# Kernel tuning notes

Hardware: AMD Instinct MI355X
Metric: run time of the kernel (lower is better)

Reference implementation:

```python
import jax, jax.numpy as jnp
import numpy as np

N = 10000      # num_nodes
E = 640000     # num edges
IN, HID, OUT = 128, 128, 128


def setup_inputs() -> dict:
    key = jax.random.key(0)
    k = jax.random.split(key, 7)
    node_features = jax.random.normal(k[0], (N, IN), dtype=jnp.float32)
    edge_index = jax.random.randint(k[1], (2, E), 0, N)
    edge_attributes = jax.random.uniform(k[2], (E,), dtype=jnp.float32)
    # GCNConv params: weight [in, out] (glorot-ish), bias [out] (zeros in PyG; use small random)
    W1 = jax.random.normal(k[3], (IN, HID), dtype=jnp.float32) * (1.0 / np.sqrt(IN))
    b1 = jnp.zeros((HID,), dtype=jnp.float32)
    W2 = jax.random.normal(k[4], (HID, OUT), dtype=jnp.float32) * (1.0 / np.sqrt(HID))
    b2 = jnp.zeros((OUT,), dtype=jnp.float32)
    return {"node_features": node_features, "edge_index": edge_index,
            "edge_attributes": edge_attributes, "W1": W1, "b1": b1, "W2": W2, "b2": b2}


def gcn_conv(x, edge_index, edge_weight, W, b, n):
    """PyG GCNConv: add self-loops (weight 1), symmetric deg^{-1/2} normalization,
    linear transform, scatter-add aggregation source->target, then bias."""
    xw = x @ W                                   # [n, out]
    row, col = edge_index[0], edge_index[1]
    loop = jnp.arange(n)
    row = jnp.concatenate([row, loop])
    col = jnp.concatenate([col, loop])
    w = jnp.concatenate([edge_weight, jnp.ones((n,), edge_weight.dtype)])
    deg = jax.ops.segment_sum(w, col, num_segments=n)
    deg_safe = jnp.where(deg > 0, deg, 1.0)
    dinv = jnp.where(deg > 0, jax.lax.rsqrt(deg_safe), 0.0)
    norm = dinv[row] * w * dinv[col]             # [E+n]
    out = jax.ops.segment_sum(norm[:, None] * xw[row], col, num_segments=n)
    return out + b


def reference(node_features, edge_index, edge_attributes, W1, b1, W2, b2):
    # Module replaces node_features with all-ones of shape (num_nodes, input_channels).
    x = jnp.ones((N, IN), dtype=node_features.dtype)
    x = jax.nn.relu(gcn_conv(x, edge_index, edge_attributes, W1, b1, N))
    x = gcn_conv(x, edge_index, edge_attributes, W2, b2, N)
    # global_mean_pool with batch=None -> mean over all nodes, shape [1, OUT]
    return jnp.mean(x, axis=0, keepdims=True)
```

## Files before the change

### kernel.cpp

```cpp
#include <hip/hip_runtime.h>

#define N_NODES 10000
#define E_EDGES 640000
#define C 128
#define NBA 128
#define NBS 128
#define NBC 63
#define CCH 160

typedef float vf4 __attribute__((ext_vector_type(4)));

__device__ __forceinline__ void lds_add(float* p, float v) {
    __hip_atomic_fetch_add(p, v, __ATOMIC_RELAXED, __HIP_MEMORY_SCOPE_WORKGROUP);
}

__global__ __launch_bounds__(512) void k_deg(const int* __restrict__ col,
                                             const float* __restrict__ w,
                                             float* __restrict__ degp) {
    __shared__ float sdeg[N_NODES];
    const int tid = threadIdx.x, bid = blockIdx.x;
    vf4 z = {0.f, 0.f, 0.f, 0.f};
    for (int i = tid; i < N_NODES / 4; i += 512) ((vf4*)sdeg)[i] = z;
    __syncthreads();
    const int epb = E_EDGES / NBA;
    const int4*   col4 = (const int4*)(col + bid * epb);
    const float4* w4   = (const float4*)(w + bid * epb);
    for (int k = tid; k < epb / 4; k += 512) {
        int4 cc = col4[k]; float4 ww = w4[k];
        lds_add(&sdeg[cc.x], ww.x);
        lds_add(&sdeg[cc.y], ww.y);
        lds_add(&sdeg[cc.z], ww.z);
        lds_add(&sdeg[cc.w], ww.w);
    }
    __syncthreads();
    float* dst = degp + (size_t)bid * N_NODES;
    for (int i = tid; i < N_NODES / 4; i += 512)
        ((vf4*)dst)[i] = ((const vf4*)sdeg)[i];
}

__global__ __launch_bounds__(256) void k_dinv(const float* __restrict__ degp,
                                              float* __restrict__ dinv,
                                              const float* __restrict__ W1,
                                              float* __restrict__ s1,
                                              float* __restrict__ g,
                                              unsigned* __restrict__ ctrl) {
    int i = blockIdx.x * 256 + threadIdx.x;
    if (i < N_NODES) {
        float d = 1.0f;
        #pragma unroll 16
        for (int b = 0; b < NBA; ++b) d += degp[(size_t)b * N_NODES + i];
        dinv[i] = rsqrtf(d);
    }
    if (blockIdx.x == 0) {
        if (threadIdx.x < C) {
            int j = threadIdx.x;
            float s = 0.0f;
            #pragma unroll 16
            for (int k = 0; k < C; ++k) s += W1[k * C + j];
            s1[j] = s;
            g[j]  = 0.0f;
        }
        if (threadIdx.x == 0) *ctrl = 0u;
    }
}

__global__ __launch_bounds__(512) void k_scatter(const int* __restrict__ row,
                                                 const int* __restrict__ col,
                                                 const float* __restrict__ w,
                                                 const float* __restrict__ dinv,
                                                 float* __restrict__ tap,
                                                 float* __restrict__ tbp) {
    __shared__ float st[N_NODES];
    const int tid = threadIdx.x;
    const bool isA = blockIdx.x < NBS;
    const int bid  = isA ? blockIdx.x : blockIdx.x - NBS;
    vf4 z = {0.f, 0.f, 0.f, 0.f};
    for (int i = tid; i < N_NODES / 4; i += 512) ((vf4*)st)[i] = z;
    __syncthreads();
    const int epb = E_EDGES / NBS;
    const int4*   row4 = (const int4*)(row + bid * epb);
    const int4*   col4 = (const int4*)(col + bid * epb);
    const float4* w4   = (const float4*)(w + bid * epb);
    if (isA) {
        for (int k = tid; k < epb / 4; k += 512) {
            int4 rr = row4[k]; int4 cc = col4[k]; float4 ww = w4[k];
            lds_add(&st[cc.x], ww.x * dinv[rr.x]);
            lds_add(&st[cc.y], ww.y * dinv[rr.y]);
            lds_add(&st[cc.z], ww.z * dinv[rr.z]);
            lds_add(&st[cc.w], ww.w * dinv[rr.w]);
        }
    } else {
        for (int k = tid; k < epb / 4; k += 512) {
            int4 rr = row4[k]; int4 cc = col4[k]; float4 ww = w4[k];
            lds_add(&st[rr.x], ww.x * dinv[cc.x]);
            lds_add(&st[rr.y], ww.y * dinv[cc.y]);
            lds_add(&st[rr.z], ww.z * dinv[cc.z]);
            lds_add(&st[rr.w], ww.w * dinv[cc.w]);
        }
    }
    __syncthreads();
    float* dst = (isA ? tap : tbp) + (size_t)bid * N_NODES;
    for (int i = tid; i < N_NODES / 4; i += 512)
        ((vf4*)dst)[i] = ((const vf4*)st)[i];
}

__global__ __launch_bounds__(512) void k_greduce(const float* __restrict__ tap,
                                                 const float* __restrict__ tbp,
                                                 const float* __restrict__ dinv,
                                                 const float* __restrict__ s1,
                                                 const float* __restrict__ b1,
                                                 const float* __restrict__ W2,
                                                 const float* __restrict__ b2,
                                                 float* __restrict__ g,
                                                 unsigned* __restrict__ ctrl,
                                                 float* __restrict__ out) {
    __shared__ float sal[CCH], sbe[CCH], sp[512];
    __shared__ int lastFlag;
    const int tid = threadIdx.x, bid = blockIdx.x;
    const int i0 = bid * CCH;
    int n = N_NODES - i0;
    n = n < 0 ? 0 : (n > CCH ? CCH : n);
    if (tid < n) {
        int i = i0 + tid;
        float ta = 0.0f;
        #pragma unroll 16
        for (int b = 0; b < NBS; ++b) ta += tap[(size_t)b * N_NODES + i];
        float di = dinv[i];
        sal[tid] = fmaf(di, ta, di * di);
    } else if (tid >= 256 && tid - 256 < n) {
        int t = tid - 256;
        int i = i0 + t;
        float tb = 0.0f;
        #pragma unroll 16
        for (int b = 0; b < NBS; ++b) tb += tbp[(size_t)b * N_NODES + i];
        float di = dinv[i];
        sbe[t] = fmaf(di, tb, di * di);
    }
    __syncthreads();
    const int j   = tid & (C - 1);
    const int sub = tid >> 7;
    float s1j = s1[j], b1j = b1[j], acc = 0.0f;
    for (int t = sub; t < n; t += 4) {
        float h = fmaf(sal[t], s1j, b1j);
        acc += sbe[t] * fmaxf(h, 0.0f);
    }
    sp[tid] = acc;
    __syncthreads();
    if (tid < C) {
        float G = sp[tid] + sp[tid + 128] + sp[tid + 256] + sp[tid + 384];
        unsafeAtomicAdd(&g[tid], G);
    }
    __syncthreads();
    if (tid == 0) {
        unsigned old = __hip_atomic_fetch_add(ctrl, 1u, __ATOMIC_ACQ_REL,
                                              __HIP_MEMORY_SCOPE_AGENT);
        lastFlag = (old == NBC - 1);
        if (lastFlag) __builtin_amdgcn_fence(__ATOMIC_ACQUIRE, "agent");
    }
    __syncthreads();
    if (lastFlag) {
        float a2 = 0.0f;
        #pragma unroll
        for (int k = sub * 32; k < sub * 32 + 32; ++k)
            a2 += g[k] * W2[k * C + j];
        sp[tid] = a2;
        __syncthreads();
        if (tid < C) {
            float r = sp[tid] + sp[tid + 128] + sp[tid + 256] + sp[tid + 384];
            out[tid] = r * (1.0f / (float)N_NODES) + b2[tid];
        }
    }
}

extern "C" void kernel_launch(void* const* d_in, const int* in_sizes, int n_in,
                              void* d_out, int out_size, void* d_ws, size_t ws_size,
                              hipStream_t stream) {
    const int*   eidx = (const int*)d_in[1];
    const int*   row  = eidx;
    const int*   col  = eidx + E_EDGES;
    const float* w    = (const float*)d_in[2];
    const float* W1   = (const float*)d_in[3];
    const float* b1   = (const float*)d_in[4];
    const float* W2   = (const float*)d_in[5];
    const float* b2   = (const float*)d_in[6];
    float* out = (float*)d_out;
    float* ws  = (float*)d_ws;

    float*    degp = ws;
    float*    tap  = degp + (size_t)NBA * N_NODES;
    float*    tbp  = tap  + (size_t)NBS * N_NODES;
    float*    dinv = tbp  + (size_t)NBS * N_NODES;
    float*    s1   = dinv + N_NODES;
    float*    g    = s1 + C;
    unsigned* ctrl = (unsigned*)(g + C);

    k_deg    <<<NBA, 512, 0, stream>>>(col, w, degp);
    k_dinv   <<<(N_NODES + 255) / 256, 256, 0, stream>>>(degp, dinv, W1, s1, g, ctrl);
    k_scatter<<<2 * NBS, 512, 0, stream>>>(row, col, w, dinv, tap, tbp);
    k_greduce<<<NBC, 512, 0, stream>>>(tap, tbp, dinv, s1, b1, W2, b2, g, ctrl, out);
}
```

Measured before the change: 49.40 us.

## Fuse dinv computation into scatter kernel with grid-wide spin barrier

Removes the separate k_dinv launch. Each of the 256 scatter blocks reduces 40 nodes' partial degrees, then all blocks wait at a device-wide atomic spin barrier before scattering. The s1/g/ctrl initialisation moves into an extra block of k_deg, and the greduce grid is doubled with half the chunk size. This saves a kernel launch and its gap, but relies on all 256 blocks being co-resident and adds spin-wait latency.

```diff
diff --git a/kernel.cpp b/kernel.cpp
--- a/kernel.cpp
+++ b/kernel.cpp
@@ -5,8 +5,9 @@
 #define C 128
 #define NBA 128
 #define NBS 128
-#define NBC 63
-#define CCH 160
+#define NBC 125
+#define CCH 80
+#define FPB 40
 
 typedef float vf4 __attribute__((ext_vector_type(4)));
 
@@ -14,11 +15,36 @@
     __hip_atomic_fetch_add(p, v, __ATOMIC_RELAXED, __HIP_MEMORY_SCOPE_WORKGROUP);
 }
 
+__device__ __forceinline__ void bar_spin(unsigned* c, unsigned tgt) {
+    __syncthreads();
+    if (threadIdx.x == 0) {
+        __hip_atomic_fetch_add(c, 1u, __ATOMIC_RELEASE, __HIP_MEMORY_SCOPE_AGENT);
+        while (__hip_atomic_load(c, __ATOMIC_ACQUIRE, __HIP_MEMORY_SCOPE_AGENT) < tgt)
+            __builtin_amdgcn_s_sleep(32);
+    }
+    __syncthreads();
+}
+
 __global__ __launch_bounds__(512) void k_deg(const int* __restrict__ col,
                                              const float* __restrict__ w,
-                                             float* __restrict__ degp) {
+                                             const float* __restrict__ W1,
+                                             float* __restrict__ degp,
+                                             float* __restrict__ s1,
+                                             float* __restrict__ g,
+                                             unsigned* __restrict__ ctrl) {
+    const int tid = threadIdx.x, bid = blockIdx.x;
+    if (bid == NBA) {
+        if (tid < C) {
+            float s = 0.0f;
+            #pragma unroll 16
+            for (int k = 0; k < C; ++k) s += W1[k * C + tid];
+            s1[tid] = s;
+            g[tid]  = 0.0f;
+        }
+        if (tid < 2) ctrl[tid * 32] = 0u;
+        return;
+    }
     __shared__ float sdeg[N_NODES];
-    const int tid = threadIdx.x, bid = blockIdx.x;
     vf4 z = {0.f, 0.f, 0.f, 0.f};
     for (int i = tid; i < N_NODES / 4; i += 512) ((vf4*)sdeg)[i] = z;
     __syncthreads();
@@ -38,45 +64,43 @@
         ((vf4*)dst)[i] = ((const vf4*)sdeg)[i];
 }
 
-__global__ __launch_bounds__(256) void k_dinv(const float* __restrict__ degp,
-                                              float* __restrict__ dinv,
-                                              const float* __restrict__ W1,
-                                              float* __restrict__ s1,
-                                              float* __restrict__ g,
-                                              unsigned* __restrict__ ctrl) {
-    int i = blockIdx.x * 256 + threadIdx.x;
-    if (i < N_NODES) {
-        float d = 1.0f;
-        #pragma unroll 16
-        for (int b = 0; b < NBA; ++b) d += degp[(size_t)b * N_NODES + i];
-        dinv[i] = rsqrtf(d);
-    }
-    if (blockIdx.x == 0) {
-        if (threadIdx.x < C) {
-            int j = threadIdx.x;
-            float s = 0.0f;
-            #pragma unroll 16
-            for (int k = 0; k < C; ++k) s += W1[k * C + j];
-            s1[j] = s;
-            g[j]  = 0.0f;
-        }
-        if (threadIdx.x == 0) *ctrl = 0u;
-    }
-}
-
 __global__ __launch_bounds__(512) void k_scatter(const int* __restrict__ row,
                                                  const int* __restrict__ col,
                                                  const float* __restrict__ w,
-                                                 const float* __restrict__ dinv,
+                                                 const float* __restrict__ degp,
+                                                 float* __restrict__ dinv,
                                                  float* __restrict__ tap,
-                                                 float* __restrict__ tbp) {
+                                                 float* __restrict__ tbp,
+                                                 unsigned* __restrict__ ctrl) {
     __shared__ float st[N_NODES];
+    __shared__ float sf[8][FPB];
     const int tid = threadIdx.x;
     const bool isA = blockIdx.x < NBS;
     const int bid  = isA ? blockIdx.x : blockIdx.x - NBS;
     vf4 z = {0.f, 0.f, 0.f, 0.f};
     for (int i = tid; i < N_NODES / 4; i += 512) ((vf4*)st)[i] = z;
-    __syncthreads();
+
+    {
+        const int i0 = blockIdx.x * FPB;
+        const int node = tid & 63;
+        const int grp  = tid >> 6;
+        if (node < FPB && i0 + node < N_NODES) {
+            float d = 0.0f;
+            #pragma unroll 16
+            for (int b = grp * 16; b < grp * 16 + 16; ++b)
+                d += degp[(size_t)b * N_NODES + i0 + node];
+            sf[grp][node] = d;
+        }
+        __syncthreads();
+        if (tid < FPB && i0 + tid < N_NODES) {
+            float d = 1.0f;
+            #pragma unroll
+            for (int gp = 0; gp < 8; ++gp) d += sf[gp][tid];
+            dinv[i0 + tid] = rsqrtf(d);
+        }
+    }
+    bar_spin(ctrl, 2 * NBS);
+
     const int epb = E_EDGES / NBS;
     const int4*   row4 = (const int4*)(row + bid * epb);
     const int4*   col4 = (const int4*)(col + bid * epb);
@@ -152,7 +176,7 @@
     }
     __syncthreads();
     if (tid == 0) {
-        unsigned old = __hip_atomic_fetch_add(ctrl, 1u, __ATOMIC_ACQ_REL,
+        unsigned old = __hip_atomic_fetch_add(ctrl + 32, 1u, __ATOMIC_ACQ_REL,
                                               __HIP_MEMORY_SCOPE_AGENT);
         lastFlag = (old == NBC - 1);
         if (lastFlag) __builtin_amdgcn_fence(__ATOMIC_ACQUIRE, "agent");
@@ -194,8 +218,7 @@
     float*    g    = s1 + C;
     unsigned* ctrl = (unsigned*)(g + C);
 
-    k_deg    <<<NBA, 512, 0, stream>>>(col, w, degp);
-    k_dinv   <<<(N_NODES + 255) / 256, 256, 0, stream>>>(degp, dinv, W1, s1, g, ctrl);
-    k_scatter<<<2 * NBS, 512, 0, stream>>>(row, col, w, dinv, tap, tbp);
+    k_deg    <<<NBA + 1, 512, 0, stream>>>(col, w, W1, degp, s1, g, ctrl);
+    k_scatter<<<2 * NBS, 512, 0, stream>>>(row, col, w, degp, dinv, tap, tbp, ctrl);
     k_greduce<<<NBC, 512, 0, stream>>>(tap, tbp, dinv, s1, b1, W2, b2, g, ctrl, out);
 }
```

Result: slower. 53.12 us (+7.5%).

## Fuse degree, dinv and scatter kernels into one kernel with atomic inter-block barriers

Applied to the files above, without the earlier changes.

Replaces the separate degree, dinv and scatter launches with a single kernel. Role-split blocks synchronise through agent-scope atomic counters that blocks spin on. The A-scatter blocks compute the partial degrees themselves, then reuse the same edge slice for the A scatter. This removes two kernel launches and their gaps, and keeps the edge data warm in cache. In exchange it adds spin-wait barriers that depend on all 335 blocks being co-resident, plus a memset to reset the counters.

```diff
diff --git a/kernel.cpp b/kernel.cpp
--- a/kernel.cpp
+++ b/kernel.cpp
@@ -3,8 +3,8 @@
 #define N_NODES 10000
 #define E_EDGES 640000
 #define C 128
-#define NBA 128
 #define NBS 128
+#define NFOLD 79
 #define NBC 63
 #define CCH 160
 
@@ -13,75 +13,80 @@
 __device__ __forceinline__ void lds_add(float* p, float v) {
     __hip_atomic_fetch_add(p, v, __ATOMIC_RELAXED, __HIP_MEMORY_SCOPE_WORKGROUP);
 }
-
-__global__ __launch_bounds__(512) void k_deg(const int* __restrict__ col,
-                                             const float* __restrict__ w,
-                                             float* __restrict__ degp) {
-    __shared__ float sdeg[N_NODES];
-    const int tid = threadIdx.x, bid = blockIdx.x;
+__device__ __forceinline__ void arrive(unsigned* c) {
+    if (threadIdx.x == 0)
+        __hip_atomic_fetch_add(c, 1u, __ATOMIC_RELEASE, __HIP_MEMORY_SCOPE_AGENT);
+}
+__device__ __forceinline__ void wait_for(unsigned* c, unsigned tgt) {
+    if (threadIdx.x == 0) {
+        while (__hip_atomic_load(c, __ATOMIC_ACQUIRE, __HIP_MEMORY_SCOPE_AGENT) < tgt)
+            __builtin_amdgcn_s_sleep(64);
+    }
+    __syncthreads();
+}
+
+__global__ __launch_bounds__(512, 4) void k_fused(
+    const int* __restrict__ row, const int* __restrict__ col,
+    const float* __restrict__ w, const float* __restrict__ W1,
+    float* __restrict__ degp, float* __restrict__ tap, float* __restrict__ tbp,
+    float* __restrict__ dinv, float* __restrict__ s1, unsigned* __restrict__ ctrl)
+{
+    __shared__ float st[N_NODES];
+    const int tid = threadIdx.x;
+    const int b = blockIdx.x;
     vf4 z = {0.f, 0.f, 0.f, 0.f};
-    for (int i = tid; i < N_NODES / 4; i += 512) ((vf4*)sdeg)[i] = z;
-    __syncthreads();
-    const int epb = E_EDGES / NBA;
-    const int4*   col4 = (const int4*)(col + bid * epb);
-    const float4* w4   = (const float4*)(w + bid * epb);
-    for (int k = tid; k < epb / 4; k += 512) {
-        int4 cc = col4[k]; float4 ww = w4[k];
-        lds_add(&sdeg[cc.x], ww.x);
-        lds_add(&sdeg[cc.y], ww.y);
-        lds_add(&sdeg[cc.z], ww.z);
-        lds_add(&sdeg[cc.w], ww.w);
-    }
-    __syncthreads();
-    float* dst = degp + (size_t)bid * N_NODES;
-    for (int i = tid; i < N_NODES / 4; i += 512)
-        ((vf4*)dst)[i] = ((const vf4*)sdeg)[i];
-}
-
-__global__ __launch_bounds__(256) void k_dinv(const float* __restrict__ degp,
-                                              float* __restrict__ dinv,
-                                              const float* __restrict__ W1,
-                                              float* __restrict__ s1,
-                                              float* __restrict__ g,
-                                              unsigned* __restrict__ ctrl) {
-    int i = blockIdx.x * 256 + threadIdx.x;
-    if (i < N_NODES) {
-        float d = 1.0f;
-        #pragma unroll 16
-        for (int b = 0; b < NBA; ++b) d += degp[(size_t)b * N_NODES + i];
-        dinv[i] = rsqrtf(d);
-    }
-    if (blockIdx.x == 0) {
-        if (threadIdx.x < C) {
-            int j = threadIdx.x;
+
+    if (b < NFOLD) {
+        float (*sf)[C] = (float(*)[C])st;
+        const int i0 = b * C;
+        if (b == 0 && tid >= 256 && tid < 256 + C) {
+            int j = tid - 256;
             float s = 0.0f;
             #pragma unroll 16
             for (int k = 0; k < C; ++k) s += W1[k * C + j];
             s1[j] = s;
-            g[j]  = 0.0f;
-        }
-        if (threadIdx.x == 0) *ctrl = 0u;
-    }
-}
-
-__global__ __launch_bounds__(512) void k_scatter(const int* __restrict__ row,
-                                                 const int* __restrict__ col,
-                                                 const float* __restrict__ w,
-                                                 const float* __restrict__ dinv,
-                                                 float* __restrict__ tap,
-                                                 float* __restrict__ tbp) {
-    __shared__ float st[N_NODES];
-    const int tid = threadIdx.x;
-    const bool isA = blockIdx.x < NBS;
-    const int bid  = isA ? blockIdx.x : blockIdx.x - NBS;
-    vf4 z = {0.f, 0.f, 0.f, 0.f};
-    for (int i = tid; i < N_NODES / 4; i += 512) ((vf4*)st)[i] = z;
-    __syncthreads();
-    const int epb = E_EDGES / NBS;
-    const int4*   row4 = (const int4*)(row + bid * epb);
-    const int4*   col4 = (const int4*)(col + bid * epb);
-    const float4* w4   = (const float4*)(w + bid * epb);
-    if (isA) {
+        }
+        wait_for(ctrl + 0, NBS);
+        const int p = tid >> 7, n = tid & (C - 1);
+        float d = 0.0f;
+        #pragma unroll 16
+        for (int bb = p * 32; bb < p * 32 + 32; ++bb)
+            d += degp[(size_t)bb * N_NODES + i0 + n];
+        sf[p][n] = d;
+        __syncthreads();
+        if (tid < C) {
+            int i = i0 + tid;
+            if (i < N_NODES) {
+                float dd = 1.0f + sf[0][tid] + sf[1][tid] + sf[2][tid] + sf[3][tid];
+                dinv[i] = rsqrtf(dd);
+            }
+        }
+        __syncthreads();
+        arrive(ctrl + 32);
+    } else if (b < NFOLD + NBS) {
+        const int bid = b - NFOLD;
+        for (int i = tid; i < N_NODES / 4; i += 512) ((vf4*)st)[i] = z;
+        __syncthreads();
+        const int epb = E_EDGES / NBS;
+        const int4*   row4 = (const int4*)(row + bid * epb);
+        const int4*   col4 = (const int4*)(col + bid * epb);
+        const float4* w4   = (const float4*)(w + bid * epb);
+        for (int k = tid; k < epb / 4; k += 512) {
+            int4 cc = col4[k]; float4 ww = w4[k];
+            lds_add(&st[cc.x], ww.x);
+            lds_add(&st[cc.y], ww.y);
+            lds_add(&st[cc.z], ww.z);
+            lds_add(&st[cc.w], ww.w);
+        }
+        __syncthreads();
+        float* dd = degp + (size_t)bid * N_NODES;
+        for (int i = tid; i < N_NODES / 4; i += 512)
+            ((vf4*)dd)[i] = ((const vf4*)st)[i];
+        __syncthreads();
+        arrive(ctrl + 0);
+        for (int i = tid; i < N_NODES / 4; i += 512)
+            ((vf4*)st)[i] = z;
+        wait_for(ctrl + 32, NFOLD);
         for (int k = tid; k < epb / 4; k += 512) {
             int4 rr = row4[k]; int4 cc = col4[k]; float4 ww = w4[k];
             lds_add(&st[cc.x], ww.x * dinv[rr.x]);
@@ -89,7 +94,18 @@
             lds_add(&st[cc.z], ww.z * dinv[rr.z]);
             lds_add(&st[cc.w], ww.w * dinv[rr.w]);
         }
+        __syncthreads();
+        float* da = tap + (size_t)bid * N_NODES;
+        for (int i = tid; i < N_NODES / 4; i += 512)
+            ((vf4*)da)[i] = ((const vf4*)st)[i];
     } else {
+        const int bid = b - NFOLD - NBS;
+        for (int i = tid; i < N_NODES / 4; i += 512) ((vf4*)st)[i] = z;
+        wait_for(ctrl + 32, NFOLD);
+        const int epb = E_EDGES / NBS;
+        const int4*   row4 = (const int4*)(row + bid * epb);
+        const int4*   col4 = (const int4*)(col + bid * epb);
+        const float4* w4   = (const float4*)(w + bid * epb);
         for (int k = tid; k < epb / 4; k += 512) {
             int4 rr = row4[k]; int4 cc = col4[k]; float4 ww = w4[k];
             lds_add(&st[rr.x], ww.x * dinv[cc.x]);
@@ -97,11 +113,11 @@
             lds_add(&st[rr.z], ww.z * dinv[cc.z]);
             lds_add(&st[rr.w], ww.w * dinv[cc.w]);
         }
-    }
-    __syncthreads();
-    float* dst = (isA ? tap : tbp) + (size_t)bid * N_NODES;
-    for (int i = tid; i < N_NODES / 4; i += 512)
-        ((vf4*)dst)[i] = ((const vf4*)st)[i];
+        __syncthreads();
+        float* db = tbp + (size_t)bid * N_NODES;
+        for (int i = tid; i < N_NODES / 4; i += 512)
+            ((vf4*)db)[i] = ((const vf4*)st)[i];
+    }
 }
 
 __global__ __launch_bounds__(512) void k_greduce(const float* __restrict__ tap,
@@ -152,7 +168,7 @@
     }
     __syncthreads();
     if (tid == 0) {
-        unsigned old = __hip_atomic_fetch_add(ctrl, 1u, __ATOMIC_ACQ_REL,
+        unsigned old = __hip_atomic_fetch_add(ctrl + 64, 1u, __ATOMIC_ACQ_REL,
                                               __HIP_MEMORY_SCOPE_AGENT);
         lastFlag = (old == NBC - 1);
         if (lastFlag) __builtin_amdgcn_fence(__ATOMIC_ACQUIRE, "agent");
@@ -187,15 +203,15 @@
     float* ws  = (float*)d_ws;
 
     float*    degp = ws;
-    float*    tap  = degp + (size_t)NBA * N_NODES;
+    float*    tap  = degp + (size_t)NBS * N_NODES;
     float*    tbp  = tap  + (size_t)NBS * N_NODES;
     float*    dinv = tbp  + (size_t)NBS * N_NODES;
     float*    s1   = dinv + N_NODES;
     float*    g    = s1 + C;
     unsigned* ctrl = (unsigned*)(g + C);
 
-    k_deg    <<<NBA, 512, 0, stream>>>(col, w, degp);
-    k_dinv   <<<(N_NODES + 255) / 256, 256, 0, stream>>>(degp, dinv, W1, s1, g, ctrl);
-    k_scatter<<<2 * NBS, 512, 0, stream>>>(row, col, w, dinv, tap, tbp);
+    (void)hipMemsetAsync(g, 0, C * sizeof(float) + 96 * sizeof(unsigned), stream);
+    k_fused  <<<NFOLD + 2 * NBS, 512, 0, stream>>>(row, col, w, W1,
+                                                   degp, tap, tbp, dinv, s1, ctrl);
     k_greduce<<<NBC, 512, 0, stream>>>(tap, tbp, dinv, s1, b1, W2, b2, g, ctrl, out);
 }
```

Result: slower. 72.25 us (+46.3%).

## Fuse reduction stages into producer kernels via last-block work stealing

Applied to the files above, without the earlier changes.

Merges the dinv computation into the degree kernel and the final reduction into the scatter kernel. The last blocks to finish spin-wait on an atomic counter and then do the reduction work, so two kernel launches and their gaps are removed. A memset zeroes the counters and the accumulator. This relies on all blocks being co-resident for the spin-wait to be safe, and the stealing blocks sit idle while they wait.

```diff
diff --git a/kernel.cpp b/kernel.cpp
--- a/kernel.cpp
+++ b/kernel.cpp
@@ -4,8 +4,10 @@
 #define E_EDGES 640000
 #define C 128
 #define NBA 128
+#define NSTEAL_D 40
+#define DCH 256
 #define NBS 128
-#define NBC 63
+#define NSTEAL_G 63
 #define CCH 160
 
 typedef float vf4 __attribute__((ext_vector_type(4)));
@@ -16,9 +18,23 @@
 
 __global__ __launch_bounds__(512) void k_deg(const int* __restrict__ col,
                                              const float* __restrict__ w,
-                                             float* __restrict__ degp) {
+                                             const float* __restrict__ W1,
+                                             float* __restrict__ degp,
+                                             float* __restrict__ dinv,
+                                             float* __restrict__ s1,
+                                             unsigned* __restrict__ ctrl) {
+    const int tid = threadIdx.x, bid = blockIdx.x;
+    if (bid == NBA) {
+        if (tid < C) {
+            float s = 0.0f;
+            #pragma unroll 16
+            for (int k = 0; k < C; ++k) s += W1[k * C + tid];
+            s1[tid] = s;
+        }
+        return;
+    }
     __shared__ float sdeg[N_NODES];
-    const int tid = threadIdx.x, bid = blockIdx.x;
+    __shared__ int ssteal;
     vf4 z = {0.f, 0.f, 0.f, 0.f};
     for (int i = tid; i < N_NODES / 4; i += 512) ((vf4*)sdeg)[i] = z;
     __syncthreads();
@@ -36,31 +52,28 @@
     float* dst = degp + (size_t)bid * N_NODES;
     for (int i = tid; i < N_NODES / 4; i += 512)
         ((vf4*)dst)[i] = ((const vf4*)sdeg)[i];
-}
-
-__global__ __launch_bounds__(256) void k_dinv(const float* __restrict__ degp,
-                                              float* __restrict__ dinv,
-                                              const float* __restrict__ W1,
-                                              float* __restrict__ s1,
-                                              float* __restrict__ g,
-                                              unsigned* __restrict__ ctrl) {
-    int i = blockIdx.x * 256 + threadIdx.x;
-    if (i < N_NODES) {
-        float d = 1.0f;
-        #pragma unroll 16
-        for (int b = 0; b < NBA; ++b) d += degp[(size_t)b * N_NODES + i];
-        dinv[i] = rsqrtf(d);
-    }
-    if (blockIdx.x == 0) {
-        if (threadIdx.x < C) {
-            int j = threadIdx.x;
-            float s = 0.0f;
+    __syncthreads();
+    if (tid == 0) {
+        unsigned old = __hip_atomic_fetch_add(ctrl, 1u, __ATOMIC_ACQ_REL,
+                                              __HIP_MEMORY_SCOPE_AGENT);
+        ssteal = (int)old - (NBA - NSTEAL_D);
+        if (ssteal >= 0 && old < NBA - 1) {
+            while (__hip_atomic_load(ctrl, __ATOMIC_ACQUIRE,
+                                     __HIP_MEMORY_SCOPE_AGENT) < NBA)
+                __builtin_amdgcn_s_sleep(16);
+        }
+    }
+    __syncthreads();
+    const int s = ssteal;
+    if (s < 0) return;
+    if (tid < DCH) {
+        int i = s * DCH + tid;
+        if (i < N_NODES) {
+            float d = 1.0f;
             #pragma unroll 16
-            for (int k = 0; k < C; ++k) s += W1[k * C + j];
-            s1[j] = s;
-            g[j]  = 0.0f;
-        }
-        if (threadIdx.x == 0) *ctrl = 0u;
+            for (int b = 0; b < NBA; ++b) d += degp[(size_t)b * N_NODES + i];
+            dinv[i] = rsqrtf(d);
+        }
     }
 }
 
@@ -68,9 +81,17 @@
                                                  const int* __restrict__ col,
                                                  const float* __restrict__ w,
                                                  const float* __restrict__ dinv,
+                                                 const float* __restrict__ s1,
+                                                 const float* __restrict__ b1,
+                                                 const float* __restrict__ W2,
+                                                 const float* __restrict__ b2,
                                                  float* __restrict__ tap,
-                                                 float* __restrict__ tbp) {
+                                                 float* __restrict__ tbp,
+                                                 float* __restrict__ g,
+                                                 unsigned* __restrict__ ctrl,
+                                                 float* __restrict__ out) {
     __shared__ float st[N_NODES];
+    __shared__ int ssteal, lastFlag;
     const int tid = threadIdx.x;
     const bool isA = blockIdx.x < NBS;
     const int bid  = isA ? blockIdx.x : blockIdx.x - NBS;
@@ -102,22 +123,24 @@
     float* dst = (isA ? tap : tbp) + (size_t)bid * N_NODES;
     for (int i = tid; i < N_NODES / 4; i += 512)
         ((vf4*)dst)[i] = ((const vf4*)st)[i];
-}
-
-__global__ __launch_bounds__(512) void k_greduce(const float* __restrict__ tap,
-                                                 const float* __restrict__ tbp,
-                                                 const float* __restrict__ dinv,
-                                                 const float* __restrict__ s1,
-                                                 const float* __restrict__ b1,
-                                                 const float* __restrict__ W2,
-                                                 const float* __restrict__ b2,
-                                                 float* __restrict__ g,
-                                                 unsigned* __restrict__ ctrl,
-                                                 float* __restrict__ out) {
-    __shared__ float sal[CCH], sbe[CCH], sp[512];
-    __shared__ int lastFlag;
-    const int tid = threadIdx.x, bid = blockIdx.x;
-    const int i0 = bid * CCH;
+    __syncthreads();
+    if (tid == 0) {
+        unsigned old = __hip_atomic_fetch_add(ctrl + 32, 1u, __ATOMIC_ACQ_REL,
+                                              __HIP_MEMORY_SCOPE_AGENT);
+        ssteal = (int)old - (2 * NBS - NSTEAL_G);
+        if (ssteal >= 0 && old < 2 * NBS - 1) {
+            while (__hip_atomic_load(ctrl + 32, __ATOMIC_ACQUIRE,
+                                     __HIP_MEMORY_SCOPE_AGENT) < 2 * NBS)
+                __builtin_amdgcn_s_sleep(16);
+        }
+    }
+    __syncthreads();
+    const int sidx = ssteal;
+    if (sidx < 0) return;
+    float* sal = st;
+    float* sbe = st + CCH;
+    float* sp  = st + 2 * CCH;
+    const int i0 = sidx * CCH;
     int n = N_NODES - i0;
     n = n < 0 ? 0 : (n > CCH ? CCH : n);
     if (tid < n) {
@@ -152,9 +175,9 @@
     }
     __syncthreads();
     if (tid == 0) {
-        unsigned old = __hip_atomic_fetch_add(ctrl, 1u, __ATOMIC_ACQ_REL,
+        unsigned old = __hip_atomic_fetch_add(ctrl + 64, 1u, __ATOMIC_ACQ_REL,
                                               __HIP_MEMORY_SCOPE_AGENT);
-        lastFlag = (old == NBC - 1);
+        lastFlag = (old == NSTEAL_G - 1);
         if (lastFlag) __builtin_amdgcn_fence(__ATOMIC_ACQUIRE, "agent");
     }
     __syncthreads();
@@ -186,16 +209,16 @@
     float* out = (float*)d_out;
     float* ws  = (float*)d_ws;
 
-    float*    degp = ws;
+    unsigned* ctrl = (unsigned*)ws;
+    float*    g    = (float*)(ctrl + 96);
+    float*    s1   = g + C;
+    float*    dinv = s1 + C;
+    float*    degp = dinv + N_NODES;
     float*    tap  = degp + (size_t)NBA * N_NODES;
     float*    tbp  = tap  + (size_t)NBS * N_NODES;
-    float*    dinv = tbp  + (size_t)NBS * N_NODES;
-    float*    s1   = dinv + N_NODES;
-    float*    g    = s1 + C;
-    unsigned* ctrl = (unsigned*)(g + C);
-
-    k_deg    <<<NBA, 512, 0, stream>>>(col, w, degp);
-    k_dinv   <<<(N_NODES + 255) / 256, 256, 0, stream>>>(degp, dinv, W1, s1, g, ctrl);
-    k_scatter<<<2 * NBS, 512, 0, stream>>>(row, col, w, dinv, tap, tbp);
-    k_greduce<<<NBC, 512, 0, stream>>>(tap, tbp, dinv, s1, b1, W2, b2, g, ctrl, out);
-}
+
+    (void)hipMemsetAsync(ws, 0, 96 * sizeof(unsigned) + C * sizeof(float), stream);
+    k_deg    <<<NBA + 1, 512, 0, stream>>>(col, w, W1, degp, dinv, s1, ctrl);
+    k_scatter<<<2 * NBS, 512, 0, stream>>>(row, col, w, dinv, s1, b1, W2, b2,
+                                           tap, tbp, g, ctrl, out);
+}
```

After: 67.10 us. 35.8% more time.
